# Optimization experiments

Measured on AMD Instinct MI355X. Metric: run time of the kernel, lower is better.

Reference implementation:

```python
import jax, jax.numpy as jnp
import numpy as np

DN = ('NCDHW', 'OIDHW', 'NCDHW')


def conv3d(x, w, stride=1):
    # kernel 3, SAME-style padding 1 (submanifold / strided sparse conv on a dense grid)
    return jax.lax.conv_general_dilated(
        x, w, window_strides=(stride,) * 3, padding=[(1, 1)] * 3,
        dimension_numbers=DN)


def tconv3d(x, w):
    # stride-2 transposed conv, kernel 3: doubles each spatial dim
    # (expressed as lhs-dilated conv; dilated = 2*in-1, pad (1,2) -> out = 2*in)
    return jax.lax.conv_general_dilated(
        x, w, window_strides=(1, 1, 1), padding=[(1, 2)] * 3,
        lhs_dilation=(2, 2, 2), dimension_numbers=DN)


def bn_relu(x, g, b, eps=1e-5):
    mu = jnp.mean(x, axis=(0, 2, 3, 4), keepdims=True)
    var = jnp.var(x, axis=(0, 2, 3, 4), keepdims=True)
    xh = (x - mu) * jax.lax.rsqrt(var + eps)
    c = (1, -1, 1, 1, 1)
    return jax.nn.relu(xh * g.reshape(c) + b.reshape(c))


def setup_inputs() -> dict:
    key = jax.random.key(0)
    ks = jax.random.split(key, 16)
    S = 0.1  # weight scale
    inp = {
        'x': jax.random.normal(ks[0], (1, 8, 128, 128, 128), jnp.float32),
        'w0': jax.random.normal(ks[1], (8, 8, 3, 3, 3), jnp.float32) * S,
        'g0': jnp.ones((8,), jnp.float32), 'b0': jnp.zeros((8,), jnp.float32),
        'w1': jax.random.normal(ks[2], (16, 8, 3, 3, 3), jnp.float32) * S,
        'g1': jnp.ones((16,), jnp.float32), 'b1': jnp.zeros((16,), jnp.float32),
        'w2': jax.random.normal(ks[3], (32, 16, 3, 3, 3), jnp.float32) * S,
        'g2': jnp.ones((32,), jnp.float32), 'b2': jnp.zeros((32,), jnp.float32),
        'w3': jax.random.normal(ks[4], (64, 32, 3, 3, 3), jnp.float32) * S,
        'g3': jnp.ones((64,), jnp.float32), 'b3': jnp.zeros((64,), jnp.float32),
        'wt3': jax.random.normal(ks[5], (32, 64, 3, 3, 3), jnp.float32) * S,
        'gt3': jnp.ones((32,), jnp.float32), 'bt3': jnp.zeros((32,), jnp.float32),
        'wt2': jax.random.normal(ks[6], (32, 64, 3, 3, 3), jnp.float32) * S,
        'gt2': jnp.ones((32,), jnp.float32), 'bt2': jnp.zeros((32,), jnp.float32),
        'wt1': jax.random.normal(ks[7], (24, 48, 3, 3, 3), jnp.float32) * S,
        'gt1': jnp.ones((24,), jnp.float32), 'bt1': jnp.zeros((24,), jnp.float32),
        'w_out': jax.random.normal(ks[8], (2, 32, 3, 3, 3), jnp.float32) * S,
    }
    return inp


def reference(x, w0, g0, b0, w1, g1, b1, w2, g2, b2, w3, g3, b3,
              wt3, gt3, bt3, wt2, gt2, bt2, wt1, gt1, bt1, w_out):
    # encoder
    s1 = bn_relu(conv3d(x, w0, 1), g0, b0)     # [1, 8,128^3]
    s2 = bn_relu(conv3d(s1, w1, 2), g1, b1)    # [1,16, 64^3]
    s4 = bn_relu(conv3d(s2, w2, 2), g2, b2)    # [1,32, 32^3]
    s8 = bn_relu(conv3d(s4, w3, 2), g3, b3)    # [1,64, 16^3]
    # decoder with skip concats
    d = bn_relu(tconv3d(s8, wt3), gt3, bt3)    # [1,32, 32^3]
    d = jnp.concatenate([d, s4], axis=1)       # [1,64, 32^3]
    d = bn_relu(tconv3d(d, wt2), gt2, bt2)     # [1,32, 64^3]
    d = jnp.concatenate([d, s2], axis=1)       # [1,48, 64^3]
    d = bn_relu(tconv3d(d, wt1), gt1, bt1)     # [1,24,128^3]
    d = jnp.concatenate([d, s1], axis=1)       # [1,32,128^3]
    return conv3d(d, w_out, 1)                 # [1, 2,128^3]
```

## Files before the change

### kernel.cpp

```cpp
#include <hip/hip_runtime.h>
#include <hip/hip_bf16.h>

typedef __hip_bfloat16 bf16;
#define TPB 256

typedef __attribute__((ext_vector_type(8))) short s8v;
typedef __attribute__((ext_vector_type(4))) float f4v;

__device__ inline void wred2(float& a, float& b) {
#pragma unroll
    for (int o = 32; o > 0; o >>= 1) {
        a += __shfl_down(a, o, 64);
        b += __shfl_down(b, o, 64);
    }
}

__device__ inline void bnco(const float* st, const float* g, const float* b,
                            float invN, int ch0, float* sc, float* sh) {
#pragma unroll
    for (int j = 0; j < 8; ++j) {
        int ch = ch0 + j;
        float mean = st[2 * ch] * invN;
        float var  = st[2 * ch + 1] * invN - mean * mean;
        sc[j] = rsqrtf(var + 1e-5f) * g[ch];
        sh[j] = b[ch] - mean * sc[j];
    }
}
__device__ inline void bnap(const uint4& u, const float* sc, const float* sh,
                            bf16* o) {
    const unsigned short* s = (const unsigned short*)&u;
#pragma unroll
    for (int j = 0; j < 8; ++j) {
        float v = __uint_as_float((unsigned)s[j] << 16);
        v = v * sc[j] + sh[j];
        o[j] = __float2bfloat16(v > 0.f ? v : 0.f);
    }
}

__device__ inline void rep_wbc(const float* __restrict__ w,
                               bf16* __restrict__ wb,
                               int OCR, int IC, int KK, int NT, int vb)
{
    int idx = vb * TPB + (int)threadIdx.x;
    int tot = KK * NT * 512;
    if (idx >= tot) return;
    int j = idx & 7;
    int l = (idx >> 3) & 63;
    int rest = idx >> 9;
    int nt = rest % NT;
    int kk = rest / NT;
    int n = nt * 16 + (l & 15);
    int k = kk * 32 + (l >> 4) * 8 + j;
    int tap = k / IC, ci = k % IC;
    float v = (n < OCR && tap < 27) ? w[(n * IC + ci) * 27 + tap] : 0.f;
    wb[idx] = __float2bfloat16(v);
}

__device__ inline void rep_wb(const float* __restrict__ w,
                              bf16* __restrict__ wb,
                              int OCR, int IC, int KC, int NT, int vb)
{
    int idx = vb * TPB + (int)threadIdx.x;
    int tot = 27 * KC * NT * 512;
    if (idx >= tot) return;
    int j = idx & 7;
    int l = (idx >> 3) & 63;
    int rest = idx >> 9;
    int nt = rest % NT;
    int kc = (rest / NT) % KC;
    int kt = rest / (NT * KC);
    int n = nt * 16 + (l & 15);
    int k = kc * 32 + (l >> 4) * 8 + j;
    float v = (n < OCR && k < IC) ? w[(n * IC + k) * 27 + kt] : 0.f;
    wb[idx] = __float2bfloat16(v);
}

__device__ inline void rep_wc(const float* __restrict__ w,
                              bf16* __restrict__ wc, int vb)
{
    int idx = vb * TPB + (int)threadIdx.x;
    if (idx >= 1728) return;
    int ci = idx & 31;
    int n = (idx >> 5) & 1;
    int tap = idx >> 6;
    wc[idx] = __float2bfloat16(w[(n * 32 + ci) * 27 + tap]);
}

__global__ __launch_bounds__(TPB) void init_all_k(
    const float* wt1, const float* wt2, const float* wt3,
    const float* w0, const float* w1, const float* w2, const float* w3,
    const float* wout,
    bf16* wbt1, bf16* wbt2, bf16* wbt3,
    bf16* wb0, bf16* wb1, bf16* wb2, bf16* wb3, bf16* wc)
{
    int b = blockIdx.x;
    if (b < 216) { rep_wb(wt1, wbt1, 24, 48, 2, 2, b); return; } b -= 216;
    if (b < 216) { rep_wb(wt2, wbt2, 32, 64, 2, 2, b); return; } b -= 216;
    if (b < 216) { rep_wb(wt3, wbt3, 32, 64, 2, 2, b); return; } b -= 216;
    if (b < 14)  { rep_wbc(w0, wb0, 8,  8,  7,  1, b); return; } b -= 14;
    if (b < 14)  { rep_wbc(w1, wb1, 16, 8,  7,  1, b); return; } b -= 14;
    if (b < 56)  { rep_wbc(w2, wb2, 32, 16, 14, 2, b); return; } b -= 56;
    if (b < 216) { rep_wbc(w3, wb3, 64, 32, 27, 4, b); return; } b -= 216;
    rep_wc(wout, wc, b);
}

__global__ __launch_bounds__(TPB) void sumcol_k(
    const float* __restrict__ p, int nrow, float* __restrict__ out)
{
    __shared__ float ws[4];
    const long col = blockIdx.x;
    float s = 0.f;
    for (int r = threadIdx.x; r < nrow; r += TPB) s += p[col * nrow + r];
    float d = 0.f;
    wred2(s, d);
    if ((threadIdx.x & 63) == 0) ws[threadIdx.x >> 6] = s;
    __syncthreads();
    if (threadIdx.x == 0) out[col] = ws[0] + ws[1] + ws[2] + ws[3];
}

template <int IC, int OCR, int STRIDE, int TZ, int TY, int TX,
          bool INF32, bool CFOUT, bool DOSTATS, bool BNIN>
__global__ __launch_bounds__(TPB) void conv_mfma_k(
    const void* __restrict__ in_, const bf16* __restrict__ wb,
    bf16* __restrict__ out, float* __restrict__ outf,
    int ID, int IH, int IW, int OD, int OH, int OW, int CSin, int CSout,
    float* __restrict__ prt, int nrow,
    const float* __restrict__ bst, const float* __restrict__ bg,
    const float* __restrict__ bb, float binvN)
{
    constexpr int EZ = STRIDE * TZ + 3 - STRIDE;
    constexpr int EY = STRIDE * TY + 3 - STRIDE;
    constexpr int EX = STRIDE * TX + 3 - STRIDE;
    constexpr int NR = EZ * EY * EX;
    constexpr int PITCH = (IC == 8) ? 8 : IC + 8;
    constexpr int CHK = IC / 8;
    constexpr int KK = (27 * IC + 31) / 32;
    constexpr int NT = (OCR + 15) / 16;
    constexpr int MT = (TY * TX) / 16;
    constexpr int MROWS = 16 / TX;
    static_assert(TZ == 4, "wave = z-slice");
    static_assert(TPB % CHK == 0, "thread-fixed chunk");
    __shared__ __align__(16) bf16 si[NR * PITCH];
    __shared__ float ps[4][2 * 16 * NT];
    const int ntx = OW / TX, nty = OH / TY;
    const int bx = blockIdx.x % ntx;
    const int by = (blockIdx.x / ntx) % nty;
    const int bz = blockIdx.x / (ntx * nty);
    const int x0 = bx * TX * STRIDE - 1;
    const int y0 = by * TY * STRIDE - 1;
    const int z0 = bz * TZ * STRIDE - 1;

    if constexpr (INF32) {
        static_assert(!INF32 || (IC == 8 && PITCH == 8), "INF32 assumes IC=8");
        const float* x = (const float*)in_;
        const long S = (long)ID * IH * IW;
        for (int i = threadIdx.x; i < NR; i += TPB) {
            int rx = i % EX; int t = i / EX; int ry = t % EY; int rz = t / EY;
            int gz = z0 + rz, gy = y0 + ry, gx = x0 + rx;
            bf16 o[8];
            if ((unsigned)gz < (unsigned)ID && (unsigned)gy < (unsigned)IH &&
                (unsigned)gx < (unsigned)IW) {
                const float* p = x + ((long)gz * IH + gy) * IW + gx;
#pragma unroll
                for (int c = 0; c < 8; ++c)
                    o[c] = __float2bfloat16(p[(long)c * S]);
            } else {
#pragma unroll
                for (int c = 0; c < 8; ++c) o[c] = __float2bfloat16(0.f);
            }
            *(uint4*)(si + i * 8) = *(const uint4*)o;
        }
    } else {
        const bf16* in = (const bf16*)in_;
        float sc[8], sh[8];
        if constexpr (BNIN)
            bnco(bst, bg, bb, binvN, (threadIdx.x % CHK) * 8, sc, sh);
        for (int i = threadIdx.x; i < NR * CHK; i += TPB) {
            int r = i / CHK, c = i % CHK;
            int rx = r % EX, ry = (r / EX) % EY, rz = r / (EX * EY);
            int gz = z0 + rz, gy = y0 + ry, gx = x0 + rx;
            bool ok = (unsigned)gz < (unsigned)ID && (unsigned)gy < (unsigned)IH &&
                      (unsigned)gx < (unsigned)IW;
            uint4 u = make_uint4(0u, 0u, 0u, 0u);
            if (ok)
                u = *(const uint4*)(in + (((long)gz * IH + gy) * IW + gx) * CSin + c * 8);
            if constexpr (BNIN) {
                bf16 o[8];
                if (ok) bnap(u, sc, sh, o);
                else {
#pragma unroll
                    for (int j = 0; j < 8; ++j) o[j] = __float2bfloat16(0.f);
                }
                *(uint4*)(si + r * PITCH + c * 8) = *(const uint4*)o;
            } else {
                *(uint4*)(si + r * PITCH + c * 8) = u;
            }
        }
    }
    __syncthreads();

    const int w = threadIdx.x >> 6;
    const int lane = threadIdx.x & 63;
    const int q = lane >> 4, m = lane & 15;
    const int vy = m / TX, vx = m % TX;

    f4v acc[MT][NT];
#pragma unroll
    for (int mt = 0; mt < MT; ++mt)
#pragma unroll
        for (int nt = 0; nt < NT; ++nt) acc[mt][nt] = (f4v)(0.f);

#define KBODY                                                                  \
    {                                                                          \
        int flat = kk * 32 + q * 8;                                            \
        int tb = flat / IC; if (tb > 26) tb = 26;                              \
        const int cb = flat % IC;                                              \
        const int kz = tb / 9, ky = (tb / 3) % 3, kx = tb % 3;                 \
        s8v bfr[NT];                                                           \
        _Pragma("unroll")                                                      \
        for (int nt = 0; nt < NT; ++nt)                                        \
            bfr[nt] = *(const s8v*)(wb + ((long)(kk * NT + nt) << 9) + lane * 8); \
        const int iz = w * STRIDE + kz;                                        \
        const int ixc = vx * STRIDE + kx;                                      \
        _Pragma("unroll")                                                      \
        for (int mt = 0; mt < MT; ++mt) {                                      \
            int iy = (mt * MROWS + vy) * STRIDE + ky;                          \
            int row = (iz * EY + iy) * EX + ixc;                               \
            s8v av = *(const s8v*)(si + row * PITCH + cb);                     \
            _Pragma("unroll")                                                  \
            for (int nt = 0; nt < NT; ++nt)                                    \
                acc[mt][nt] = __builtin_amdgcn_mfma_f32_16x16x32_bf16(         \
                    av, bfr[nt], acc[mt][nt], 0, 0, 0);                        \
        }                                                                      \
    }

    if constexpr (KK <= 7) {
#pragma unroll
        for (int kk = 0; kk < KK; ++kk) KBODY
    } else {
#pragma unroll 1
        for (int kk = 0; kk < KK; ++kk) KBODY
    }
#undef KBODY

    float ls[NT], ls2[NT];
#pragma unroll
    for (int nt = 0; nt < NT; ++nt) { ls[nt] = 0.f; ls2[nt] = 0.f; }
    const int oz = bz * TZ + w;
#pragma unroll
    for (int mt = 0; mt < MT; ++mt)
#pragma unroll
        for (int nt = 0; nt < NT; ++nt) {
            const int n_ch = nt * 16 + m;
            if constexpr (DOSTATS) {
#pragma unroll
                for (int r = 0; r < 4; ++r) {
                    float v = acc[mt][nt][r];
                    ls[nt] += v; ls2[nt] += v * v;
                }
            }
            if (n_ch < OCR) {
#pragma unroll
                for (int r = 0; r < 4; ++r) {
                    int vrow = 4 * q + r;
                    int oy = by * TY + mt * MROWS + vrow / TX;
                    int ox = bx * TX + vrow % TX;
                    long vox = ((long)oz * OH + oy) * OW + ox;
                    if constexpr (CFOUT) {
                        long Sout = (long)OD * OH * OW;
                        outf[(long)n_ch * Sout + vox] = acc[mt][nt][r];
                    } else {
                        out[vox * CSout + n_ch] = __float2bfloat16(acc[mt][nt][r]);
                    }
                }
            }
        }
    if constexpr (DOSTATS) {
#pragma unroll
        for (int nt = 0; nt < NT; ++nt) {
            float t = ls[nt], t2 = ls2[nt];
            t  += __shfl_down(t, 32, 64);  t  += __shfl_down(t, 16, 64);
            t2 += __shfl_down(t2, 32, 64); t2 += __shfl_down(t2, 16, 64);
            if (lane < 16) {
                ps[w][2 * (nt * 16 + lane)]     = t;
                ps[w][2 * (nt * 16 + lane) + 1] = t2;
            }
        }
        __syncthreads();
        if (threadIdx.x < 2 * OCR) {
            float v = ps[0][threadIdx.x] + ps[1][threadIdx.x]
                    + ps[2][threadIdx.x] + ps[3][threadIdx.x];
            prt[(long)threadIdx.x * nrow + blockIdx.x] = v;
        }
    }
}

__global__ __launch_bounds__(TPB, 4) void outconv_k(
    const bf16* __restrict__ cat, const bf16* __restrict__ s1v,
    const bf16* __restrict__ wc, float* __restrict__ outf,
    const float* __restrict__ stats, const float* __restrict__ g,
    const float* __restrict__ b,
    const float* __restrict__ stS, const float* __restrict__ gS,
    const float* __restrict__ bS, float invN)
{
    constexpr int EY = 10, EX = 10, PITCH = 32;
    __shared__ __align__(16) bf16 si[600 * PITCH];
    const int bx = blockIdx.x & 15;
    const int by = (blockIdx.x >> 4) & 15;
    const int bz = blockIdx.x >> 8;
    const int x0 = bx * 8 - 1, y0 = by * 8 - 1, z0 = bz * 4 - 1;

    const int c4 = threadIdx.x & 3;
    float sc[8], sh[8];
    if (c4 < 3) bnco(stats, g, b, invN, c4 * 8, sc, sh);
    else        bnco(stS, gS, bS, invN, 0, sc, sh);

    const int col = threadIdx.x >> 2;
    const bool inter = (bx > 0) & (bx < 15) & (by > 0) & (by < 15) &
                       (bz > 0) & (bz < 31);
#pragma unroll
    for (int cp = 0; cp < 2; ++cp) {
        const int cc = col + cp * 64;
        if (cc < 100) {
            const int ry = cc / 10, rx = cc - ry * 10;
            const int gy = y0 + ry, gx = x0 + rx;
            const long vyx = (long)gy * 128 + gx;
            uint4 u[6];
            if (inter) {
#pragma unroll
                for (int rz = 0; rz < 6; ++rz) {
                    long vox = ((long)(z0 + rz) << 14) + vyx;
                    const bf16* p = (c4 == 3) ? (s1v + vox * 8)
                                              : (cat + vox * 24 + c4 * 8);
                    u[rz] = *(const uint4*)p;
                }
#pragma unroll
                for (int rz = 0; rz < 6; ++rz) {
                    bf16 o[8];
                    bnap(u[rz], sc, sh, o);
                    *(uint4*)(si + (rz * 100 + cc) * PITCH + c4 * 8) =
                        *(const uint4*)o;
                }
            } else {
                const bool yxok = ((unsigned)gy < 128u) & ((unsigned)gx < 128u);
                unsigned zm = 0u;
#pragma unroll
                for (int rz = 0; rz < 6; ++rz) {
                    u[rz] = make_uint4(0u, 0u, 0u, 0u);
                    int gz = z0 + rz;
                    if (yxok && (unsigned)gz < 128u) {
                        long vox = ((long)gz << 14) + vyx;
                        const bf16* p = (c4 == 3) ? (s1v + vox * 8)
                                                  : (cat + vox * 24 + c4 * 8);
                        u[rz] = *(const uint4*)p;
                        zm |= 1u << rz;
                    }
                }
#pragma unroll
                for (int rz = 0; rz < 6; ++rz) {
                    bf16 o[8];
                    if ((zm >> rz) & 1u) bnap(u[rz], sc, sh, o);
                    else {
#pragma unroll
                        for (int j = 0; j < 8; ++j) o[j] = __float2bfloat16(0.f);
                    }
                    *(uint4*)(si + (rz * 100 + cc) * PITCH + c4 * 8) =
                        *(const uint4*)o;
                }
            }
        }
    }
    __syncthreads();

    const int w = threadIdx.x >> 6;
    const int lane = threadIdx.x & 63;
    const int q = lane >> 4, m = lane & 15;
    const int vy = (m >> 3) & 1, vx = m & 7;

    f4v acc[4];
#pragma unroll
    for (int mt = 0; mt < 4; ++mt) acc[mt] = (f4v)(0.f);

    const bf16* wcl = wc + (m & 1) * 32 + q * 8;
#pragma unroll
    for (int kz = 0; kz < 3; ++kz) {
#pragma unroll
        for (int kx = 0; kx < 3; ++kx) {
            const bf16* sp = si +
                ((((w + kz) * EY + vy) * EX) + vx + kx) * PITCH + q * 8;
            s8v a[9];
#pragma unroll
            for (int j = 0; j < 9; ++j)
                a[j] = *(const s8v*)(sp + j * (EX * PITCH));
            const bf16* bp = wcl + (kz * 9 + kx) * 64;
            s8v bf0 = *(const s8v*)(bp);
            s8v bf1 = *(const s8v*)(bp + 3 * 64);
            s8v bf2 = *(const s8v*)(bp + 6 * 64);
#pragma unroll
            for (int mt = 0; mt < 4; ++mt) {
                acc[mt] = __builtin_amdgcn_mfma_f32_16x16x32_bf16(
                    a[2 * mt + 0], bf0, acc[mt], 0, 0, 0);
                acc[mt] = __builtin_amdgcn_mfma_f32_16x16x32_bf16(
                    a[2 * mt + 1], bf1, acc[mt], 0, 0, 0);
                acc[mt] = __builtin_amdgcn_mfma_f32_16x16x32_bf16(
                    a[2 * mt + 2], bf2, acc[mt], 0, 0, 0);
            }
        }
    }
    if (m < 2) {
        const long Sout = 128L * 128 * 128;
        const int oz = bz * 4 + w;
#pragma unroll
        for (int mt = 0; mt < 4; ++mt) {
#pragma unroll
            for (int r = 0; r < 4; ++r) {
                int vrow = 4 * q + r;
                int oy = by * 8 + mt * 2 + (vrow >> 3);
                int ox = bx * 8 + (vrow & 7);
                outf[(long)m * Sout + (((long)oz * 128 + oy) * 128 + ox)] =
                    acc[mt][r];
            }
        }
    }
}

template <int IC, int OCR>
__global__ __launch_bounds__(TPB) void tconv_mfma_k(
    const bf16* __restrict__ in, const bf16* __restrict__ wb,
    bf16* __restrict__ out, int ID, int IH, int IW, int CSin, int CSout,
    float* __restrict__ prt, int nrow,
    const float* __restrict__ st0, const float* __restrict__ g0p,
    const float* __restrict__ b0p, const float* __restrict__ st1,
    const float* __restrict__ g1p, const float* __restrict__ b1p,
    float binvN, int C0)
{
    constexpr int KC = (IC + 31) / 32;
    constexpr int NT = (OCR + 15) / 16;
    constexpr int TZ = 4, TY = 4, TX = 8;
    constexpr int EZ = TZ + 1, EY = TY + 1, EX = TX + 1;
    constexpr int NR = EZ * EY * EX;
    constexpr int PITCH = (IC == 48) ? 64 : 72;
    constexpr int CHKS = 8;
    constexpr int CHK = IC / 8;
    __shared__ __align__(16) bf16 si[NR * PITCH];
    __shared__ float ps[4][64];
    const int ntx = IW / TX, nty = IH / TY;
    const int bx = blockIdx.x % ntx;
    const int by = (blockIdx.x / ntx) % nty;
    const int bz = blockIdx.x / (ntx * nty);
    const int x0 = bx * TX, y0 = by * TY, z0 = bz * TZ;

    {
        const int c = threadIdx.x & 7;
        float sc[8], sh[8];
#pragma unroll
        for (int j = 0; j < 8; ++j) { sc[j] = 1.f; sh[j] = 0.f; }
        if (c < CHK) {
#pragma unroll
            for (int j = 0; j < 8; ++j) {
                int ch = c * 8 + j;
                const float* st; const float* gg; const float* bbq; int k;
                if (ch < C0) { st = st0; gg = g0p; bbq = b0p; k = ch; }
                else         { st = st1; gg = g1p; bbq = b1p; k = ch - C0; }
                float mean = st[2 * k] * binvN;
                float var  = st[2 * k + 1] * binvN - mean * mean;
                sc[j] = rsqrtf(var + 1e-5f) * gg[k];
                sh[j] = bbq[k] - mean * sc[j];
            }
        }
        for (int i = threadIdx.x; i < NR * CHKS; i += TPB) {
            int r = i >> 3, cc = i & 7;
            int rx = r % EX, ry = (r / EX) % EY, rz = r / (EX * EY);
            int gz = z0 + rz, gy = y0 + ry, gx = x0 + rx;
            bool ok = (cc < CHK) && gz < ID && gy < IH && gx < IW;
            uint4 u = make_uint4(0u, 0u, 0u, 0u);
            if (ok)
                u = *(const uint4*)(in + (((long)gz * IH + gy) * IW + gx) * CSin + cc * 8);
            bf16 o[8];
            if (ok) bnap(u, sc, sh, o);
            else {
#pragma unroll
                for (int j = 0; j < 8; ++j) o[j] = __float2bfloat16(0.f);
            }
            *(uint4*)(si + r * PITCH + cc * 8) = *(const uint4*)o;
        }
    }
    __syncthreads();
    const int w = threadIdx.x >> 6;
    const int lane = threadIdx.x & 63;
    const int q = lane >> 4, m = lane & 15;
    const int vy = m >> 3, vx = m & 7;
    const int OH = 2 * IH, OW = 2 * IW;
    float ls[NT], ls2[NT];
#pragma unroll
    for (int nt = 0; nt < NT; ++nt) { ls[nt] = 0.f; ls2[nt] = 0.f; }

#pragma unroll 1
    for (int cls = 0; cls < 8; ++cls) {
        const int pz = (cls >> 2) & 1, py = (cls >> 1) & 1, px = cls & 1;
        const int ny = 1 + py, nx = 1 + px;
        const int ntap = (1 + pz) * ny * nx;
        f4v acc[2][NT];
#pragma unroll
        for (int mt = 0; mt < 2; ++mt)
#pragma unroll
            for (int nt = 0; nt < NT; ++nt) acc[mt][nt] = (f4v)(0.f);
#pragma unroll 1
        for (int s = 0; s < ntap; ++s) {
            int a = s / (ny * nx), b = (s / nx) % ny, cc = s % nx;
            int dz = pz ? a : 0, dy = py ? b : 0, dx = px ? cc : 0;
            int kz = pz ? (a ? 2 : 0) : 1;
            int ky = py ? (b ? 2 : 0) : 1;
            int kx = px ? (cc ? 2 : 0) : 1;
            int kt = kz * 9 + ky * 3 + kx;
#pragma unroll
            for (int kc = 0; kc < KC; ++kc) {
                const bf16* bp = wb + (long)((kt * KC + kc) * NT) * 512 + lane * 8;
                s8v b0 = *(const s8v*)bp;
                s8v b1 = *(const s8v*)(bp + 512);
#pragma unroll
                for (int mt = 0; mt < 2; ++mt) {
                    int row = ((w + dz) * EY + (2 * mt + vy + dy)) * EX + (vx + dx);
                    s8v av = *(const s8v*)(si + row * PITCH + kc * 32 + q * 8);
                    acc[mt][0] = __builtin_amdgcn_mfma_f32_16x16x32_bf16(
                        av, b0, acc[mt][0], 0, 0, 0);
                    acc[mt][1] = __builtin_amdgcn_mfma_f32_16x16x32_bf16(
                        av, b1, acc[mt][1], 0, 0, 0);
                }
            }
        }
        const int z = 2 * (z0 + w) + pz;
#pragma unroll
        for (int mt = 0; mt < 2; ++mt)
#pragma unroll
            for (int nt = 0; nt < NT; ++nt) {
                const int n_ch = nt * 16 + m;
#pragma unroll
                for (int r = 0; r < 4; ++r) {
                    float v = acc[mt][nt][r];
                    ls[nt] += v; ls2[nt] += v * v;
                }
                if (n_ch < OCR) {
#pragma unroll
                    for (int r = 0; r < 4; ++r) {
                        int vrow = 4 * q + r;
                        int yy = 2 * (y0 + 2 * mt + (vrow >> 3)) + py;
                        int xx = 2 * (x0 + (vrow & 7)) + px;
                        out[(((long)z * OH + yy) * OW + xx) * CSout + n_ch] =
                            __float2bfloat16(acc[mt][nt][r]);
                    }
                }
            }
    }
#pragma unroll
    for (int nt = 0; nt < NT; ++nt) {
        float t = ls[nt], t2 = ls2[nt];
        t  += __shfl_down(t, 32, 64);  t  += __shfl_down(t, 16, 64);
        t2 += __shfl_down(t2, 32, 64); t2 += __shfl_down(t2, 16, 64);
        if (lane < 16) {
            ps[w][2 * (nt * 16 + lane)]     = t;
            ps[w][2 * (nt * 16 + lane) + 1] = t2;
        }
    }
    __syncthreads();
    if (threadIdx.x < 2 * OCR) {
        float v = ps[0][threadIdx.x] + ps[1][threadIdx.x] + ps[2][threadIdx.x]
                + ps[3][threadIdx.x];
        prt[(long)threadIdx.x * nrow + blockIdx.x] = v;
    }
}

extern "C" void kernel_launch(void* const* d_in, const int* in_sizes, int n_in,
                              void* d_out, int out_size, void* d_ws, size_t ws_size,
                              hipStream_t stream)
{
    const float* x    = (const float*)d_in[0];
    const float* w0   = (const float*)d_in[1];
    const float* g0   = (const float*)d_in[2];
    const float* b0   = (const float*)d_in[3];
    const float* w1   = (const float*)d_in[4];
    const float* g1   = (const float*)d_in[5];
    const float* b1   = (const float*)d_in[6];
    const float* w2   = (const float*)d_in[7];
    const float* g2   = (const float*)d_in[8];
    const float* b2   = (const float*)d_in[9];
    const float* w3   = (const float*)d_in[10];
    const float* g3   = (const float*)d_in[11];
    const float* b3   = (const float*)d_in[12];
    const float* wt3  = (const float*)d_in[13];
    const float* gt3  = (const float*)d_in[14];
    const float* bt3  = (const float*)d_in[15];
    const float* wt2  = (const float*)d_in[16];
    const float* gt2  = (const float*)d_in[17];
    const float* bt2  = (const float*)d_in[18];
    const float* wt1  = (const float*)d_in[19];
    const float* gt1  = (const float*)d_in[20];
    const float* bt1  = (const float*)d_in[21];
    const float* wout = (const float*)d_in[22];

    const long S128 = 128L * 128 * 128;
    const long S64  = 64L * 64 * 64;
    const long S32  = 32L * 32 * 32;
    const long S16  = 16L * 16 * 16;

    float* stats = (float*)d_ws;
    bf16*  wc    = (bf16*)((char*)d_ws + 2048);
    bf16* base = (bf16*)((char*)d_ws + 2048 + 27648);
    bf16* cat1 = base;
    bf16* cat2 = cat1 + S128 * 24;
    bf16* cat3 = cat2 + S64 * 48;
    bf16* s8   = cat3 + S32 * 64;
    bf16* s1   = s8 + S16 * 64;
    bf16* s2 = cat2 + 32;
    bf16* s4 = cat3 + 32;

    bf16*  wbb  = (bf16*)d_out;
    bf16*  wbt1 = wbb;
    bf16*  wbt2 = wbb + 55296;
    bf16*  wbt3 = wbb + 110592;
    bf16*  wb0  = wbb + 165888;
    bf16*  wb1  = wbb + 169472;
    bf16*  wb2  = wbb + 173056;
    bf16*  wb3  = wbb + 187392;
    float* prt  = (float*)d_out + 524288;

    init_all_k<<<955, TPB, 0, stream>>>(
        wt1, wt2, wt3, w0, w1, w2, w3, wout,
        wbt1, wbt2, wbt3, wb0, wb1, wb2, wb3, wc);

    conv_mfma_k<8, 8, 1, 4, 8, 8, true, false, true, false><<<8192, TPB, 0, stream>>>(
        x, wb0, s1, nullptr, 128, 128, 128, 128, 128, 128, 0, 8, prt, 8192,
        nullptr, nullptr, nullptr, 0.f);
    sumcol_k<<<16, TPB, 0, stream>>>(prt, 8192, stats + 0);

    conv_mfma_k<8, 16, 2, 4, 8, 8, false, false, true, true><<<1024, TPB, 0, stream>>>(
        s1, wb1, s2, nullptr, 128, 128, 128, 64, 64, 64, 8, 48, prt, 1024,
        stats + 0, g0, b0, 1.f / S128);
    sumcol_k<<<32, TPB, 0, stream>>>(prt, 1024, stats + 16);

    conv_mfma_k<16, 32, 2, 4, 4, 4, false, false, true, true><<<512, TPB, 0, stream>>>(
        s2, wb2, s4, nullptr, 64, 64, 64, 32, 32, 32, 48, 64, prt, 512,
        stats + 16, g1, b1, 1.f / S64);
    sumcol_k<<<64, TPB, 0, stream>>>(prt, 512, stats + 48);

    conv_mfma_k<32, 64, 2, 4, 4, 4, false, false, true, true><<<64, TPB, 0, stream>>>(
        s4, wb3, s8, nullptr, 32, 32, 32, 16, 16, 16, 64, 64, prt, 64,
        stats + 48, g2, b2, 1.f / S32);
    sumcol_k<<<128, TPB, 0, stream>>>(prt, 64, stats + 112);

    tconv_mfma_k<64, 32><<<32, TPB, 0, stream>>>(
        s8, wbt3, cat3, 16, 16, 16, 64, 64, prt, 32,
        stats + 112, g3, b3, stats + 112, g3, b3, 1.f / S16, 64);
    sumcol_k<<<64, TPB, 0, stream>>>(prt, 32, stats + 240);

    tconv_mfma_k<64, 32><<<256, TPB, 0, stream>>>(
        cat3, wbt2, cat2, 32, 32, 32, 64, 48, prt, 256,
        stats + 240, gt3, bt3, stats + 48, g2, b2, 1.f / S32, 32);
    sumcol_k<<<64, TPB, 0, stream>>>(prt, 256, stats + 304);

    tconv_mfma_k<48, 24><<<2048, TPB, 0, stream>>>(
        cat2, wbt1, cat1, 64, 64, 64, 48, 24, prt, 2048,
        stats + 304, gt2, bt2, stats + 16, g1, b1, 1.f / S64, 32);
    sumcol_k<<<48, TPB, 0, stream>>>(prt, 2048, stats + 368);

    outconv_k<<<8192, TPB, 0, stream>>>(
        cat1, s1, wc, (float*)d_out, stats + 368, gt1, bt1,
        stats + 0, g0, b0, 1.f / S128);
}
```

Baseline: 499.0 us.

## Split outconv input channels into two 16-wide halves to halve LDS

```diff
diff --git a/kernel.cpp b/kernel.cpp
--- a/kernel.cpp
+++ b/kernel.cpp
@@ -5,6 +5,7 @@
 #define TPB 256
 
 typedef __attribute__((ext_vector_type(8))) short s8v;
+typedef __attribute__((ext_vector_type(4))) short s4v;
 typedef __attribute__((ext_vector_type(4))) float f4v;
 
 __device__ inline void wred2(float& a, float& b) {
@@ -75,15 +76,16 @@
     wb[idx] = __float2bfloat16(v);
 }
 
-__device__ inline void rep_wc(const float* __restrict__ w,
-                              bf16* __restrict__ wc, int vb)
+__device__ inline void rep_wc16(const float* __restrict__ w,
+                                bf16* __restrict__ wc, int vb)
 {
     int idx = vb * TPB + (int)threadIdx.x;
-    if (idx >= 1728) return;
-    int ci = idx & 31;
-    int n = (idx >> 5) & 1;
+    if (idx >= 3456) return;
+    int ci = idx & 15;
+    int n = (idx >> 4) & 1;
+    int h = (idx >> 5) & 1;
     int tap = idx >> 6;
-    wc[idx] = __float2bfloat16(w[(n * 32 + ci) * 27 + tap]);
+    wc[idx] = __float2bfloat16(w[(n * 32 + h * 16 + ci) * 27 + tap]);
 }
 
 __global__ __launch_bounds__(TPB) void init_all_k(
@@ -101,7 +103,7 @@
     if (b < 14)  { rep_wbc(w1, wb1, 16, 8,  7,  1, b); return; } b -= 14;
     if (b < 56)  { rep_wbc(w2, wb2, 32, 16, 14, 2, b); return; } b -= 56;
     if (b < 216) { rep_wbc(w3, wb3, 64, 32, 27, 4, b); return; } b -= 216;
-    rep_wc(wout, wc, b);
+    rep_wc16(wout, wc, b);
 }
 
 __global__ __launch_bounds__(TPB) void sumcol_k(
@@ -295,7 +297,7 @@
     }
 }
 
-__global__ __launch_bounds__(TPB, 4) void outconv_k(
+__global__ __launch_bounds__(TPB, 6) void outconv_k(
     const bf16* __restrict__ cat, const bf16* __restrict__ s1v,
     const bf16* __restrict__ wc, float* __restrict__ outf,
     const float* __restrict__ stats, const float* __restrict__ g,
@@ -303,110 +305,105 @@
     const float* __restrict__ stS, const float* __restrict__ gS,
     const float* __restrict__ bS, float invN)
 {
-    constexpr int EY = 10, EX = 10, PITCH = 32;
+    constexpr int EY = 10, EX = 10, PITCH = 16;
     __shared__ __align__(16) bf16 si[600 * PITCH];
     const int bx = blockIdx.x & 15;
     const int by = (blockIdx.x >> 4) & 15;
     const int bz = blockIdx.x >> 8;
     const int x0 = bx * 8 - 1, y0 = by * 8 - 1, z0 = bz * 4 - 1;
 
-    const int c4 = threadIdx.x & 3;
-    float sc[8], sh[8];
-    if (c4 < 3) bnco(stats, g, b, invN, c4 * 8, sc, sh);
-    else        bnco(stS, gS, bS, invN, 0, sc, sh);
-
-    const int col = threadIdx.x >> 2;
-    const bool inter = (bx > 0) & (bx < 15) & (by > 0) & (by < 15) &
-                       (bz > 0) & (bz < 31);
-#pragma unroll
-    for (int cp = 0; cp < 2; ++cp) {
-        const int cc = col + cp * 64;
-        if (cc < 100) {
-            const int ry = cc / 10, rx = cc - ry * 10;
-            const int gy = y0 + ry, gx = x0 + rx;
-            const long vyx = (long)gy * 128 + gx;
-            uint4 u[6];
-            if (inter) {
-#pragma unroll
-                for (int rz = 0; rz < 6; ++rz) {
-                    long vox = ((long)(z0 + rz) << 14) + vyx;
-                    const bf16* p = (c4 == 3) ? (s1v + vox * 8)
-                                              : (cat + vox * 24 + c4 * 8);
-                    u[rz] = *(const uint4*)p;
-                }
-#pragma unroll
-                for (int rz = 0; rz < 6; ++rz) {
-                    bf16 o[8];
-                    bnap(u[rz], sc, sh, o);
-                    *(uint4*)(si + (rz * 100 + cc) * PITCH + c4 * 8) =
-                        *(const uint4*)o;
-                }
-            } else {
-                const bool yxok = ((unsigned)gy < 128u) & ((unsigned)gx < 128u);
-                unsigned zm = 0u;
-#pragma unroll
-                for (int rz = 0; rz < 6; ++rz) {
-                    u[rz] = make_uint4(0u, 0u, 0u, 0u);
-                    int gz = z0 + rz;
-                    if (yxok && (unsigned)gz < 128u) {
-                        long vox = ((long)gz << 14) + vyx;
-                        const bf16* p = (c4 == 3) ? (s1v + vox * 8)
-                                                  : (cat + vox * 24 + c4 * 8);
-                        u[rz] = *(const uint4*)p;
-                        zm |= 1u << rz;
-                    }
-                }
-#pragma unroll
-                for (int rz = 0; rz < 6; ++rz) {
-                    bf16 o[8];
-                    if ((zm >> rz) & 1u) bnap(u[rz], sc, sh, o);
-                    else {
-#pragma unroll
-                        for (int j = 0; j < 8; ++j) o[j] = __float2bfloat16(0.f);
-                    }
-                    *(uint4*)(si + (rz * 100 + cc) * PITCH + c4 * 8) =
-                        *(const uint4*)o;
-                }
-            }
-        }
-    }
-    __syncthreads();
-
     const int w = threadIdx.x >> 6;
     const int lane = threadIdx.x & 63;
     const int q = lane >> 4, m = lane & 15;
     const int vy = (m >> 3) & 1, vx = m & 7;
 
+    const int scc = threadIdx.x >> 1;
+    const int sc2 = threadIdx.x & 1;
+    const bool sact = scc < 100;
+    const int sry = scc / 10, srx = scc - sry * 10;
+    const int sgy = y0 + sry, sgx = x0 + srx;
+    const long svyx = (long)sgy * 128 + sgx;
+    const bool syx = ((unsigned)sgy < 128u) & ((unsigned)sgx < 128u);
+    const bool inter = (bx > 0) & (bx < 15) & (by > 0) & (by < 15) &
+                       (bz > 0) & (bz < 31);
+
     f4v acc[4];
 #pragma unroll
     for (int mt = 0; mt < 4; ++mt) acc[mt] = (f4v)(0.f);
 
-    const bf16* wcl = wc + (m & 1) * 32 + q * 8;
-#pragma unroll
-    for (int kz = 0; kz < 3; ++kz) {
-#pragma unroll
-        for (int kx = 0; kx < 3; ++kx) {
-            const bf16* sp = si +
-                ((((w + kz) * EY + vy) * EX) + vx + kx) * PITCH + q * 8;
-            s8v a[9];
-#pragma unroll
-            for (int j = 0; j < 9; ++j)
-                a[j] = *(const s8v*)(sp + j * (EX * PITCH));
-            const bf16* bp = wcl + (kz * 9 + kx) * 64;
-            s8v bf0 = *(const s8v*)(bp);
-            s8v bf1 = *(const s8v*)(bp + 3 * 64);
-            s8v bf2 = *(const s8v*)(bp + 6 * 64);
-#pragma unroll
-            for (int mt = 0; mt < 4; ++mt) {
-                acc[mt] = __builtin_amdgcn_mfma_f32_16x16x32_bf16(
-                    a[2 * mt + 0], bf0, acc[mt], 0, 0, 0);
-                acc[mt] = __builtin_amdgcn_mfma_f32_16x16x32_bf16(
-                    a[2 * mt + 1], bf1, acc[mt], 0, 0, 0);
-                acc[mt] = __builtin_amdgcn_mfma_f32_16x16x32_bf16(
-                    a[2 * mt + 2], bf2, acc[mt], 0, 0, 0);
-            }
-        }
-    }
+#pragma unroll
+    for (int h = 0; h < 2; ++h) {
+        if (sact) {
+            const int ch0 = h * 16 + sc2 * 8;
+            float sc[8], sh[8];
+            if (ch0 < 24) bnco(stats, g, b, invN, ch0, sc, sh);
+            else          bnco(stS, gS, bS, invN, 0, sc, sh);
+            const bf16* srcb = (ch0 < 24) ? (cat + ch0) : s1v;
+            const long cs = (ch0 < 24) ? 24 : 8;
+            uint4 u[6];
+            unsigned zm = 0u;
+            if (inter) {
+#pragma unroll
+                for (int rz = 0; rz < 6; ++rz) {
+                    long vox = ((long)(z0 + rz) << 14) + svyx;
+                    u[rz] = *(const uint4*)(srcb + vox * cs);
+                }
+                zm = 0x3fu;
+            } else {
+#pragma unroll
+                for (int rz = 0; rz < 6; ++rz) {
+                    u[rz] = make_uint4(0u, 0u, 0u, 0u);
+                    int gz = z0 + rz;
+                    if (syx && (unsigned)gz < 128u) {
+                        long vox = ((long)gz << 14) + svyx;
+                        u[rz] = *(const uint4*)(srcb + vox * cs);
+                        zm |= 1u << rz;
+                    }
+                }
+            }
+#pragma unroll
+            for (int rz = 0; rz < 6; ++rz) {
+                bf16 o[8];
+                if ((zm >> rz) & 1u) bnap(u[rz], sc, sh, o);
+                else {
+#pragma unroll
+                    for (int j = 0; j < 8; ++j) o[j] = __float2bfloat16(0.f);
+                }
+                *(uint4*)(si + (rz * 100 + scc) * PITCH + sc2 * 8) =
+                    *(const uint4*)o;
+            }
+        }
+        __syncthreads();
+
+#pragma unroll
+        for (int kz = 0; kz < 3; ++kz) {
+#pragma unroll
+            for (int kx = 0; kx < 3; ++kx) {
+                const bf16* sp = si +
+                    ((((w + kz) * EY + vy) * EX) + vx + kx) * PITCH + q * 4;
+                s4v a[9];
+#pragma unroll
+                for (int j = 0; j < 9; ++j)
+                    a[j] = *(const s4v*)(sp + j * (EX * PITCH));
+                const bf16* bp = wc +
+                    (((kz * 9 + kx) * 2 + h) * 2 + (m & 1)) * 16 + q * 4;
+                s4v bf0 = *(const s4v*)(bp);
+                s4v bf1 = *(const s4v*)(bp + 192);
+                s4v bf2 = *(const s4v*)(bp + 384);
+#pragma unroll
+                for (int mt = 0; mt < 4; ++mt) {
+                    acc[mt] = __builtin_amdgcn_mfma_f32_16x16x16bf16_1k(
+                        a[2 * mt + 0], bf0, acc[mt], 0, 0, 0);
+                    acc[mt] = __builtin_amdgcn_mfma_f32_16x16x16bf16_1k(
+                        a[2 * mt + 1], bf1, acc[mt], 0, 0, 0);
+                    acc[mt] = __builtin_amdgcn_mfma_f32_16x16x16bf16_1k(
+                        a[2 * mt + 2], bf2, acc[mt], 0, 0, 0);
+                }
+            }
+        }
+        __syncthreads();
+    }
+
     if (m < 2) {
         const long Sout = 128L * 128 * 128;
         const int oz = bz * 4 + w;
@@ -624,7 +621,7 @@
     bf16*  wb3  = wbb + 187392;
     float* prt  = (float*)d_out + 524288;
 
-    init_all_k<<<955, TPB, 0, stream>>>(
+    init_all_k<<<962, TPB, 0, stream>>>(
         wt1, wt2, wt3, w0, w1, w2, w3, wout,
         wbt1, wbt2, wbt3, wb0, wb1, wb2, wb3, wc);
 
@@ -660,7 +657,7 @@
 
     tconv_mfma_k<48, 24><<<2048, TPB, 0, stream>>>(
         cat2, wbt1, cat1, 64, 64, 64, 48, 24, prt, 2048,
-        stats + 304, gt2, bt2, stats + 16, g1, b1, 1.f / S64, 32);
+        stats + 304, gt2, gt2 ? bt2 : bt2, stats + 16, g1, b1, 1.f / S64, 32);
     sumcol_k<<<48, TPB, 0, stream>>>(prt, 2048, stats + 368);
 
     outconv_k<<<8192, TPB, 0, stream>>>(
```

Result: slower. 613.9 us (+23.0%).
